# Kernel tuning notes

Measured on AMD Instinct MI355X. Metric: run time of the kernel, lower is better.

The kernel has to match this reference:

```python
import jax, jax.numpy as jnp
import numpy as np

B, C, H, W = 32, 3, 512, 512
OUT = (64, 64)  # (out_grid[0]=Nx, out_grid[1]=Ny)
SMALL = 1e-4


def setup_inputs() -> dict:
    key = jax.random.key(0)
    k1, k2 = jax.random.split(key, 2)
    X = jax.random.normal(k1, (B, C, H, W), dtype=jnp.float32)
    fan_in = C * H * W
    # localization net: flatten + dense(5); scaled so p ~ N(0,1) and exp(p) is stable
    W_loc = jax.random.normal(k2, (fan_in, 5), dtype=jnp.float32) / np.float32(np.sqrt(fan_in))
    b_loc = jnp.zeros((5,), dtype=jnp.float32)
    return {"X": X, "W_loc": W_loc, "b_loc": b_loc}


def reference(X, W_loc, b_loc):
    Bn = X.shape[0]
    # locnet: p = flatten(X) @ W_loc + b_loc  -> [B, 5]
    p = X.reshape(Bn, -1) @ W_loc + b_loc

    N = min(OUT)
    gx = OUT[0] * (p[:, 0] + 1.0) / 2.0          # [B]
    gy = OUT[1] * (p[:, 1] + 1.0) / 2.0          # [B]
    sigma2 = jnp.exp(p[:, 2])                    # [B]
    delta = jnp.exp(p[:, 3]) * (max(W, H) - 1) / (N - 1.0)  # [B]
    gamma = jnp.exp(p[:, 4])                     # [B]

    i1 = jnp.arange(OUT[0], dtype=jnp.float32)   # [Nx]
    i2 = jnp.arange(OUT[1], dtype=jnp.float32)   # [Ny]
    a = jnp.arange(W, dtype=jnp.float32)         # [W]
    b = jnp.arange(H, dtype=jnp.float32)         # [H]

    mx = gx[:, None] + delta[:, None] * (i1 - N / 2.0 - 0.5)  # [B, Nx]
    my = gy[:, None] + delta[:, None] * (i2 - N / 2.0 - 0.5)  # [B, Ny]

    Fx = jnp.exp(-((a - mx[:, :, None]) ** 2) / (2.0 * sigma2[:, None, None]))  # [B,Nx,W]
    Fx = Fx / (Fx.sum(axis=-1, keepdims=True) + SMALL)
    Fy = jnp.exp(-((b - my[:, :, None]) ** 2) / (2.0 * sigma2[:, None, None]))  # [B,Ny,H]
    Fy = Fy / (Fy.sum(axis=-1, keepdims=True) + SMALL)

    # glimpse read: gamma * Fy @ X @ Fx^T, done as batched contractions
    Fyx = jnp.einsum('bnh,bchw->bcnw', Fy, X)        # [B,C,Ny,W]
    out = jnp.einsum('bcnw,bmw->bcnm', Fyx, Fx)      # [B,C,Ny,Nx]
    return gamma[:, None, None, None] * out
```

## Files before the change

### kernel.cpp

```cpp
#include <hip/hip_runtime.h>
#include <math.h>

#define B_ 32
#define C_ 3
#define H_ 512
#define W_ 512
#define NOUT 64
#define FAN (C_*H_*W_)

#define CHUNKS 192
#define CELEMS (FAN / CHUNKS)
#define BGROUPS 4
#define NREP 8

#define PFLOATS 2048
#define FXH_U 0
#define FXL_U 1048576
#define FYH_U 2097152
#define FYL_U 3145728

typedef __bf16 bf16x8 __attribute__((ext_vector_type(8)));
typedef float f32x4 __attribute__((ext_vector_type(4)));

__device__ __forceinline__ unsigned short f2bf(float f) {
    unsigned int u = __float_as_uint(f);
    u = (u + 0x7FFFu + ((u >> 16) & 1u)) >> 16;
    return (unsigned short)u;
}
__device__ __forceinline__ float bf2f(unsigned short h) {
    return __uint_as_float(((unsigned int)h) << 16);
}
__device__ __forceinline__ unsigned int cvt_pk_bf16(float lo, float hi) {
    unsigned int r;
    asm("v_cvt_pk_bf16_f32 %0, %1, %2" : "=v"(r) : "v"(lo), "v"(hi));
    return r;
}

__global__ __launch_bounds__(256) void k_locnet(const float* __restrict__ X,
                                                const float* __restrict__ Wl,
                                                float* __restrict__ ws) {
    const int chunk = blockIdx.x;
    const int b0 = blockIdx.y * 8;
    const int t = threadIdx.x;
    const int rep = chunk & (NREP - 1);

    float acc[8][5] = {};
    const size_t base = (size_t)chunk * CELEMS;

    for (int k = t; k < CELEMS / 4; k += 256) {
        const size_t i0 = base + (size_t)k * 4;
        const float4* W4 = (const float4*)(Wl + i0 * 5);
        float4 w0 = W4[0], w1 = W4[1], w2 = W4[2], w3 = W4[3], w4 = W4[4];
        float wv[20] = {w0.x, w0.y, w0.z, w0.w,
                        w1.x, w1.y, w1.z, w1.w,
                        w2.x, w2.y, w2.z, w2.w,
                        w3.x, w3.y, w3.z, w3.w,
                        w4.x, w4.y, w4.z, w4.w};
        #pragma unroll
        for (int bb = 0; bb < 8; bb++) {
            float4 x = *(const float4*)(X + (size_t)(b0 + bb) * FAN + i0);
            float xv[4] = {x.x, x.y, x.z, x.w};
            #pragma unroll
            for (int e = 0; e < 4; e++)
                #pragma unroll
                for (int j = 0; j < 5; j++)
                    acc[bb][j] += xv[e] * wv[e * 5 + j];
        }
    }

    #pragma unroll
    for (int off = 32; off > 0; off >>= 1)
        #pragma unroll
        for (int bb = 0; bb < 8; bb++)
            #pragma unroll
            for (int j = 0; j < 5; j++)
                acc[bb][j] += __shfl_down(acc[bb][j], off);

    __shared__ float sred[4][40];
    const int wave = t >> 6, lane = t & 63;
    if (lane == 0) {
        #pragma unroll
        for (int bb = 0; bb < 8; bb++)
            #pragma unroll
            for (int j = 0; j < 5; j++)
                sred[wave][bb * 5 + j] = acc[bb][j];
    }
    __syncthreads();
    if (t < 40) {
        float s = sred[0][t] + sred[1][t] + sred[2][t] + sred[3][t];
        atomicAdd(&ws[rep * 256 + b0 * 5 + t], s);
    }
}

__global__ __launch_bounds__(256) void k_filters(const float* __restrict__ bl,
                                                 float* __restrict__ ws,
                                                 float* __restrict__ out) {
    const int n = blockIdx.x;
    const int b = blockIdx.y;
    const int which = blockIdx.z;
    const int t = threadIdx.x;

    {
        const int bid = blockIdx.x + NOUT * (blockIdx.y + B_ * blockIdx.z);
        if (t < 24) {
            float4 z = make_float4(0.f, 0.f, 0.f, 0.f);
            ((float4*)out)[(size_t)bid * 24 + t] = z;
        }
    }

    float p0 = bl[0], p1 = bl[1], p2 = bl[2], p3 = bl[3];
    #pragma unroll
    for (int rep = 0; rep < NREP; rep++) {
        const float* pr = ws + rep * 256 + b * 5;
        p0 += pr[0]; p1 += pr[1]; p2 += pr[2]; p3 += pr[3];
    }

    const float g = (which == 0) ? 32.f * (p0 + 1.f) : 32.f * (p1 + 1.f);
    const float sigma2 = expf(p2);
    const float inv2s = 0.5f / sigma2;
    const float delta = expf(p3) * (511.0f / 63.0f);
    const float mean = g + delta * ((float)n - 32.5f);

    float d0 = (float)t - mean;
    float f0 = expf(-d0 * d0 * inv2s);
    float d1 = (float)(t + 256) - mean;
    float f1 = expf(-d1 * d1 * inv2s);

    float s = f0 + f1;
    #pragma unroll
    for (int off = 32; off > 0; off >>= 1) s += __shfl_down(s, off);
    __shared__ float sred[4];
    __shared__ float stot;
    const int wave = t >> 6, lane = t & 63;
    if (lane == 0) sred[wave] = s;
    __syncthreads();
    if (t == 0) stot = sred[0] + sred[1] + sred[2] + sred[3] + 1e-4f;
    __syncthreads();
    const float scale = 1.0f / stot;

    unsigned short* wsu = (unsigned short*)(ws + PFLOATS);
    unsigned short* dstH = wsu + (which ? FYH_U : FXH_U) + ((size_t)b * NOUT + n) * 512;
    unsigned short* dstL = wsu + (which ? FYL_U : FXL_U) + ((size_t)b * NOUT + n) * 512;

    float v0 = f0 * scale;
    unsigned short h0 = f2bf(v0);
    dstH[t] = h0;
    dstL[t] = f2bf(v0 - bf2f(h0));
    float v1 = f1 * scale;
    unsigned short h1 = f2bf(v1);
    dstH[t + 256] = h1;
    dstL[t + 256] = f2bf(v1 - bf2f(h1));
}

#define KC 64
#define PITCH 72
#define TSZ (64 * PITCH)

__global__ __launch_bounds__(256) void k_glimpse(const float* __restrict__ X,
                                                 const float* __restrict__ bl,
                                                 const float* __restrict__ ws,
                                                 float* __restrict__ out) {
    const int hc = blockIdx.x;
    const int bc = blockIdx.y;
    const int b = bc / 3;
    const int t = threadIdx.x;
    const int lane = t & 63;
    const int wv = t >> 6;
    const int l15 = lane & 15;
    const int quad = lane >> 4;
    const int hbase = hc * 64;

    __shared__ __align__(16) unsigned short lds[4 * TSZ];
    unsigned short* Xh = lds;
    unsigned short* Xl = lds + TSZ;
    unsigned short* Fh = lds + 2 * TSZ;
    unsigned short* Fl = lds + 3 * TSZ;

    const float* Xp = X + (size_t)bc * (H_ * W_) + (size_t)hbase * W_;
    const unsigned short* wsu = (const unsigned short*)(ws + PFLOATS);
    const unsigned short* FxHp = wsu + FXH_U + (size_t)b * NOUT * 512;
    const unsigned short* FxLp = wsu + FXL_U + (size_t)b * NOUT * 512;
    const unsigned short* FyHp = wsu + FYH_U + (size_t)b * NOUT * 512;
    const unsigned short* FyLp = wsu + FYL_U + (size_t)b * NOUT * 512;

    f32x4 acc[4] = {};

    for (int wt = 0; wt < 8; wt++) {
        const int wbase = wt * KC;
        #pragma unroll
        for (int k4 = 0; k4 < 4; k4++) {
            int idx = t + 256 * k4;
            int row = idx >> 4;
            int c4 = (idx & 15) * 4;
            float4 xv = *(const float4*)(Xp + (size_t)row * W_ + wbase + c4);
            unsigned int h01 = cvt_pk_bf16(xv.x, xv.y);
            unsigned int h23 = cvt_pk_bf16(xv.z, xv.w);
            float r0 = __uint_as_float(h01 << 16);
            float r1 = __uint_as_float(h01 & 0xffff0000u);
            float r2 = __uint_as_float(h23 << 16);
            float r3 = __uint_as_float(h23 & 0xffff0000u);
            unsigned int l01 = cvt_pk_bf16(xv.x - r0, xv.y - r1);
            unsigned int l23 = cvt_pk_bf16(xv.z - r2, xv.w - r3);
            int o = row * PITCH + c4;
            *(uint2*)&Xh[o] = make_uint2(h01, h23);
            *(uint2*)&Xl[o] = make_uint2(l01, l23);
        }
        #pragma unroll
        for (int i = 0; i < 2; i++) {
            int idx = t + 256 * i;
            int row = idx >> 3;
            int c8 = (idx & 7) * 8;
            uint4 hv = *(const uint4*)(FxHp + (size_t)row * 512 + wbase + c8);
            uint4 lv = *(const uint4*)(FxLp + (size_t)row * 512 + wbase + c8);
            *(uint4*)&Fh[row * PITCH + c8] = hv;
            *(uint4*)&Fl[row * PITCH + c8] = lv;
        }
        __syncthreads();
        #pragma unroll
        for (int ks = 0; ks < 2; ks++) {
            const int ko = ks * 32 + quad * 8;
            bf16x8 ah = *(const bf16x8*)&Xh[(16 * wv + l15) * PITCH + ko];
            bf16x8 al = *(const bf16x8*)&Xl[(16 * wv + l15) * PITCH + ko];
            #pragma unroll
            for (int mt = 0; mt < 4; mt++) {
                bf16x8 bh = *(const bf16x8*)&Fh[(16 * mt + l15) * PITCH + ko];
                bf16x8 bl2 = *(const bf16x8*)&Fl[(16 * mt + l15) * PITCH + ko];
                acc[mt] = __builtin_amdgcn_mfma_f32_16x16x32_bf16(ah, bh, acc[mt], 0, 0, 0);
                acc[mt] = __builtin_amdgcn_mfma_f32_16x16x32_bf16(al, bh, acc[mt], 0, 0, 0);
                acc[mt] = __builtin_amdgcn_mfma_f32_16x16x32_bf16(ah, bl2, acc[mt], 0, 0, 0);
            }
        }
        __syncthreads();
    }

    #pragma unroll
    for (int mt = 0; mt < 4; mt++) {
        float g0 = acc[mt][0], g1 = acc[mt][1], g2 = acc[mt][2], g3 = acc[mt][3];
        unsigned int h01 = cvt_pk_bf16(g0, g1);
        unsigned int h23 = cvt_pk_bf16(g2, g3);
        float r0 = __uint_as_float(h01 << 16);
        float r1 = __uint_as_float(h01 & 0xffff0000u);
        float r2 = __uint_as_float(h23 << 16);
        float r3 = __uint_as_float(h23 & 0xffff0000u);
        unsigned int l01 = cvt_pk_bf16(g0 - r0, g1 - r1);
        unsigned int l23 = cvt_pk_bf16(g2 - r2, g3 - r3);
        int m = 16 * mt + l15;
        int h = 16 * wv + quad * 4;
        int o = m * PITCH + h;
        *(uint2*)&Xh[o] = make_uint2(h01, h23);
        *(uint2*)&Xl[o] = make_uint2(l01, l23);
    }

    #pragma unroll
    for (int i = 0; i < 2; i++) {
        int idx = t + 256 * i;
        int row = idx >> 3;
        int c8 = (idx & 7) * 8;
        uint4 hv = *(const uint4*)(FyHp + (size_t)row * 512 + hbase + c8);
        uint4 lv = *(const uint4*)(FyLp + (size_t)row * 512 + hbase + c8);
        *(uint4*)&Fh[row * PITCH + c8] = hv;
        *(uint4*)&Fl[row * PITCH + c8] = lv;
    }
    __syncthreads();

    f32x4 p[4] = {};
    #pragma unroll
    for (int ks = 0; ks < 2; ks++) {
        const int ko = ks * 32 + quad * 8;
        bf16x8 yh = *(const bf16x8*)&Fh[(16 * wv + l15) * PITCH + ko];
        bf16x8 yl = *(const bf16x8*)&Fl[(16 * wv + l15) * PITCH + ko];
        #pragma unroll
        for (int mt = 0; mt < 4; mt++) {
            bf16x8 gh = *(const bf16x8*)&Xh[(16 * mt + l15) * PITCH + ko];
            bf16x8 gl = *(const bf16x8*)&Xl[(16 * mt + l15) * PITCH + ko];
            p[mt] = __builtin_amdgcn_mfma_f32_16x16x32_bf16(yh, gh, p[mt], 0, 0, 0);
            p[mt] = __builtin_amdgcn_mfma_f32_16x16x32_bf16(yl, gh, p[mt], 0, 0, 0);
            p[mt] = __builtin_amdgcn_mfma_f32_16x16x32_bf16(yh, gl, p[mt], 0, 0, 0);
        }
    }

    float p4 = bl[4];
    #pragma unroll
    for (int rep = 0; rep < NREP; rep++) p4 += ws[rep * 256 + b * 5 + 4];
    const float gamma = expf(p4);

    float* outp = out + (size_t)bc * (NOUT * NOUT);
    #pragma unroll
    for (int mt = 0; mt < 4; mt++)
        #pragma unroll
        for (int r = 0; r < 4; r++) {
            int n = 16 * wv + quad * 4 + r;
            int m = 16 * mt + l15;
            atomicAdd(&outp[n * NOUT + m], gamma * p[mt][r]);
        }
}

extern "C" void kernel_launch(void* const* d_in, const int* in_sizes, int n_in,
                              void* d_out, int out_size, void* d_ws, size_t ws_size,
                              hipStream_t stream) {
    const float* X  = (const float*)d_in[0];
    const float* Wl = (const float*)d_in[1];
    const float* bl = (const float*)d_in[2];
    float* out = (float*)d_out;
    float* ws  = (float*)d_ws;

    hipMemsetAsync(ws, 0, PFLOATS * sizeof(float), stream);

    k_locnet<<<dim3(CHUNKS, BGROUPS), 256, 0, stream>>>(X, Wl, ws);
    k_filters<<<dim3(NOUT, B_, 2), 256, 0, stream>>>(bl, ws, out);
    k_glimpse<<<dim3(8, B_ * C_), 256, 0, stream>>>(X, bl, ws, out);
}
```

Before: 205.6 us.

## Prefetch next tile into registers in glimpse and drop atomics/memset for locnet partials

The glimpse kernel now loads the next X and Fx tiles (and finally the Fy tile) into registers before the MFMA loop, so global loads overlap with compute. Locnet writes per-chunk partial sums instead of atomics, which removes the workspace memset launch; the filters kernel reduces the 192 partials and precomputes gamma. Filter stores are packed as 32-bit pairs. This costs extra registers in glimpse and more partial reads in the filters kernel.

```diff
diff --git a/kernel.cpp b/kernel.cpp
--- a/kernel.cpp
+++ b/kernel.cpp
@@ -11,9 +11,10 @@
 #define CHUNKS 192
 #define CELEMS (FAN / CHUNKS)
 #define BGROUPS 4
-#define NREP 8
-
-#define PFLOATS 2048
+
+#define PPART_STRIDE 160
+#define GAMMA_OFF (CHUNKS * PPART_STRIDE)
+#define PFLOATS 32768
 #define FXH_U 0
 #define FXL_U 1048576
 #define FYH_U 2097152
@@ -42,7 +43,6 @@
     const int chunk = blockIdx.x;
     const int b0 = blockIdx.y * 8;
     const int t = threadIdx.x;
-    const int rep = chunk & (NREP - 1);
 
     float acc[8][5] = {};
     const size_t base = (size_t)chunk * CELEMS;
@@ -88,7 +88,7 @@
     __syncthreads();
     if (t < 40) {
         float s = sred[0][t] + sred[1][t] + sred[2][t] + sred[3][t];
-        atomicAdd(&ws[rep * 256 + b0 * 5 + t], s);
+        ws[(size_t)chunk * PPART_STRIDE + b0 * 5 + t] = s;
     }
 }
 
@@ -103,17 +103,34 @@
     {
         const int bid = blockIdx.x + NOUT * (blockIdx.y + B_ * blockIdx.z);
         if (t < 24) {
-            float4 z = make_float4(0.f, 0.f, 0.f, 0.f);
-            ((float4*)out)[(size_t)bid * 24 + t] = z;
-        }
-    }
-
-    float p0 = bl[0], p1 = bl[1], p2 = bl[2], p3 = bl[3];
-    #pragma unroll
-    for (int rep = 0; rep < NREP; rep++) {
-        const float* pr = ws + rep * 256 + b * 5;
-        p0 += pr[0]; p1 += pr[1]; p2 += pr[2]; p3 += pr[3];
-    }
+            ((float4*)out)[(size_t)bid * 24 + t] = make_float4(0.f, 0.f, 0.f, 0.f);
+        }
+    }
+
+    float pj[5] = {0.f, 0.f, 0.f, 0.f, 0.f};
+    if (t < CHUNKS) {
+        const float* pr = ws + (size_t)t * PPART_STRIDE + b * 5;
+        #pragma unroll
+        for (int j = 0; j < 5; j++) pj[j] = pr[j];
+    }
+    #pragma unroll
+    for (int off = 32; off > 0; off >>= 1)
+        #pragma unroll
+        for (int j = 0; j < 5; j++) pj[j] += __shfl_down(pj[j], off);
+
+    __shared__ float spart[4][5];
+    __shared__ float pfin[5];
+    const int wave = t >> 6, lane = t & 63;
+    if (lane == 0) {
+        #pragma unroll
+        for (int j = 0; j < 5; j++) spart[wave][j] = pj[j];
+    }
+    __syncthreads();
+    if (t < 5) pfin[t] = spart[0][t] + spart[1][t] + spart[2][t] + spart[3][t] + bl[t];
+    __syncthreads();
+
+    const float p0 = pfin[0], p1 = pfin[1], p2 = pfin[2], p3 = pfin[3];
+    if (which == 0 && n == 0 && t == 0) ws[GAMMA_OFF + b] = expf(pfin[4]);
 
     const float g = (which == 0) ? 32.f * (p0 + 1.f) : 32.f * (p1 + 1.f);
     const float sigma2 = expf(p2);
@@ -121,9 +138,9 @@
     const float delta = expf(p3) * (511.0f / 63.0f);
     const float mean = g + delta * ((float)n - 32.5f);
 
-    float d0 = (float)t - mean;
+    float d0 = (float)(2 * t) - mean;
     float f0 = expf(-d0 * d0 * inv2s);
-    float d1 = (float)(t + 256) - mean;
+    float d1 = (float)(2 * t + 1) - mean;
     float f1 = expf(-d1 * d1 * inv2s);
 
     float s = f0 + f1;
@@ -131,7 +148,6 @@
     for (int off = 32; off > 0; off >>= 1) s += __shfl_down(s, off);
     __shared__ float sred[4];
     __shared__ float stot;
-    const int wave = t >> 6, lane = t & 63;
     if (lane == 0) sred[wave] = s;
     __syncthreads();
     if (t == 0) stot = sred[0] + sred[1] + sred[2] + sred[3] + 1e-4f;
@@ -139,25 +155,44 @@
     const float scale = 1.0f / stot;
 
     unsigned short* wsu = (unsigned short*)(ws + PFLOATS);
-    unsigned short* dstH = wsu + (which ? FYH_U : FXH_U) + ((size_t)b * NOUT + n) * 512;
-    unsigned short* dstL = wsu + (which ? FYL_U : FXL_U) + ((size_t)b * NOUT + n) * 512;
+    unsigned int* dstH = (unsigned int*)(wsu + (which ? FYH_U : FXH_U) + ((size_t)b * NOUT + n) * 512);
+    unsigned int* dstL = (unsigned int*)(wsu + (which ? FYL_U : FXL_U) + ((size_t)b * NOUT + n) * 512);
 
     float v0 = f0 * scale;
+    float v1 = f1 * scale;
     unsigned short h0 = f2bf(v0);
-    dstH[t] = h0;
-    dstL[t] = f2bf(v0 - bf2f(h0));
-    float v1 = f1 * scale;
     unsigned short h1 = f2bf(v1);
-    dstH[t + 256] = h1;
-    dstL[t + 256] = f2bf(v1 - bf2f(h1));
+    unsigned short l0 = f2bf(v0 - bf2f(h0));
+    unsigned short l1 = f2bf(v1 - bf2f(h1));
+    dstH[t] = (unsigned int)h0 | ((unsigned int)h1 << 16);
+    dstL[t] = (unsigned int)l0 | ((unsigned int)l1 << 16);
 }
 
 #define KC 64
 #define PITCH 72
 #define TSZ (64 * PITCH)
 
+#define LOAD_X(wt_) do {                                                      \
+    const int wbase_ = (wt_) * KC;                                            \
+    _Pragma("unroll")                                                         \
+    for (int k4 = 0; k4 < 4; k4++) {                                          \
+        int idx_ = t + 256 * k4;                                              \
+        int row_ = idx_ >> 4;                                                 \
+        int c4_ = (idx_ & 15) * 4;                                            \
+        xr[k4] = *(const float4*)(Xp + (size_t)row_ * W_ + wbase_ + c4_);     \
+    } } while (0)
+
+#define LOAD_F(Hp_, Lp_, coff_) do {                                          \
+    _Pragma("unroll")                                                         \
+    for (int i_ = 0; i_ < 2; i_++) {                                          \
+        int idx_ = t + 256 * i_;                                              \
+        int row_ = idx_ >> 3;                                                 \
+        int c8_ = (idx_ & 7) * 8;                                             \
+        fhr[i_] = *(const uint4*)((Hp_) + (size_t)row_ * 512 + (coff_) + c8_);\
+        flr[i_] = *(const uint4*)((Lp_) + (size_t)row_ * 512 + (coff_) + c8_);\
+    } } while (0)
+
 __global__ __launch_bounds__(256) void k_glimpse(const float* __restrict__ X,
-                                                 const float* __restrict__ bl,
                                                  const float* __restrict__ ws,
                                                  float* __restrict__ out) {
     const int hc = blockIdx.x;
@@ -183,24 +218,28 @@
     const unsigned short* FyHp = wsu + FYH_U + (size_t)b * NOUT * 512;
     const unsigned short* FyLp = wsu + FYL_U + (size_t)b * NOUT * 512;
 
+    float4 xr[4];
+    uint4 fhr[2], flr[2];
+    LOAD_X(0);
+    LOAD_F(FxHp, FxLp, 0);
+
     f32x4 acc[4] = {};
 
     for (int wt = 0; wt < 8; wt++) {
-        const int wbase = wt * KC;
         #pragma unroll
         for (int k4 = 0; k4 < 4; k4++) {
             int idx = t + 256 * k4;
             int row = idx >> 4;
             int c4 = (idx & 15) * 4;
-            float4 xv = *(const float4*)(Xp + (size_t)row * W_ + wbase + c4);
-            unsigned int h01 = cvt_pk_bf16(xv.x, xv.y);
-            unsigned int h23 = cvt_pk_bf16(xv.z, xv.w);
+            float4 v = xr[k4];
+            unsigned int h01 = cvt_pk_bf16(v.x, v.y);
+            unsigned int h23 = cvt_pk_bf16(v.z, v.w);
             float r0 = __uint_as_float(h01 << 16);
             float r1 = __uint_as_float(h01 & 0xffff0000u);
             float r2 = __uint_as_float(h23 << 16);
             float r3 = __uint_as_float(h23 & 0xffff0000u);
-            unsigned int l01 = cvt_pk_bf16(xv.x - r0, xv.y - r1);
-            unsigned int l23 = cvt_pk_bf16(xv.z - r2, xv.w - r3);
+            unsigned int l01 = cvt_pk_bf16(v.x - r0, v.y - r1);
+            unsigned int l23 = cvt_pk_bf16(v.z - r2, v.w - r3);
             int o = row * PITCH + c4;
             *(uint2*)&Xh[o] = make_uint2(h01, h23);
             *(uint2*)&Xl[o] = make_uint2(l01, l23);
@@ -210,12 +249,18 @@
             int idx = t + 256 * i;
             int row = idx >> 3;
             int c8 = (idx & 7) * 8;
-            uint4 hv = *(const uint4*)(FxHp + (size_t)row * 512 + wbase + c8);
-            uint4 lv = *(const uint4*)(FxLp + (size_t)row * 512 + wbase + c8);
-            *(uint4*)&Fh[row * PITCH + c8] = hv;
-            *(uint4*)&Fl[row * PITCH + c8] = lv;
+            *(uint4*)&Fh[row * PITCH + c8] = fhr[i];
+            *(uint4*)&Fl[row * PITCH + c8] = flr[i];
         }
         __syncthreads();
+
+        if (wt < 7) {
+            LOAD_X(wt + 1);
+            LOAD_F(FxHp, FxLp, (wt + 1) * KC);
+        } else {
+            LOAD_F(FyHp, FyLp, hbase);
+        }
+
         #pragma unroll
         for (int ks = 0; ks < 2; ks++) {
             const int ko = ks * 32 + quad * 8;
@@ -256,10 +301,8 @@
         int idx = t + 256 * i;
         int row = idx >> 3;
         int c8 = (idx & 7) * 8;
-        uint4 hv = *(const uint4*)(FyHp + (size_t)row * 512 + hbase + c8);
-        uint4 lv = *(const uint4*)(FyLp + (size_t)row * 512 + hbase + c8);
-        *(uint4*)&Fh[row * PITCH + c8] = hv;
-        *(uint4*)&Fl[row * PITCH + c8] = lv;
+        *(uint4*)&Fh[row * PITCH + c8] = fhr[i];
+        *(uint4*)&Fl[row * PITCH + c8] = flr[i];
     }
     __syncthreads();
 
@@ -279,11 +322,7 @@
         }
     }
 
-    float p4 = bl[4];
-    #pragma unroll
-    for (int rep = 0; rep < NREP; rep++) p4 += ws[rep * 256 + b * 5 + 4];
-    const float gamma = expf(p4);
-
+    const float gamma = ws[GAMMA_OFF + b];
     float* outp = out + (size_t)bc * (NOUT * NOUT);
     #pragma unroll
     for (int mt = 0; mt < 4; mt++)
@@ -304,9 +343,7 @@
     float* out = (float*)d_out;
     float* ws  = (float*)d_ws;
 
-    hipMemsetAsync(ws, 0, PFLOATS * sizeof(float), stream);
-
     k_locnet<<<dim3(CHUNKS, BGROUPS), 256, 0, stream>>>(X, Wl, ws);
     k_filters<<<dim3(NOUT, B_, 2), 256, 0, stream>>>(bl, ws, out);
-    k_glimpse<<<dim3(8, B_ * C_), 256, 0, stream>>>(X, bl, ws, out);
-}
+    k_glimpse<<<dim3(8, B_ * C_), 256, 0, stream>>>(X, ws, out);
+}
```

Result: slower. 222.1 us (+8.0%).
